# Kernel optimization log

Hardware: AMD Instinct MI355X
Metric: run time of the kernel (lower is better)

The kernel has to match this reference:

```python
import jax, jax.numpy as jnp
import numpy as np

NUM_USERS = 4000
NUM_LOCAS = 4000
D = 128            # embedding_dynamic_size
K = 64             # kg embedding dim
KG_ROWS = 5000
T = 2048           # number of events
IN_RNN = D + 1 + K # rnn input size (KG=True)
PRED_IN = NUM_USERS + NUM_LOCAS + 2 * D + K
PRED_OUT = NUM_LOCAS + D + K
EPS = 1e-12


def setup_inputs() -> dict:
    key = jax.random.key(0)
    ks = jax.random.split(key, 20)
    s = 0.05
    f32 = jnp.float32
    return {
        "embedding": jax.random.normal(ks[0], (NUM_USERS + NUM_LOCAS, D), f32),
        "events_int": jax.random.randint(ks[1], (T, 5), 0, 4000, dtype=jnp.int32),
        "delta_u": jax.random.uniform(ks[2], (T,), f32),
        "delta_l": jax.random.uniform(ks[3], (T,), f32),
        "kg": jax.random.normal(ks[4], (KG_ROWS, K), f32) * s,
        "w_ih_u": jax.random.normal(ks[5], (D, IN_RNN), f32) * s,
        "w_hh_u": jax.random.normal(ks[6], (D, D), f32) * s,
        "b_ih_u": jax.random.normal(ks[7], (D,), f32) * s,
        "b_hh_u": jax.random.normal(ks[8], (D,), f32) * s,
        "w_ih_l": jax.random.normal(ks[9], (D, IN_RNN), f32) * s,
        "w_hh_l": jax.random.normal(ks[10], (D, D), f32) * s,
        "b_ih_l": jax.random.normal(ks[11], (D,), f32) * s,
        "b_hh_l": jax.random.normal(ks[12], (D,), f32) * s,
        "proj_w": jax.random.normal(ks[13], (D, 1), f32) * s,
        "proj_b": jax.random.normal(ks[14], (D,), f32) * s,
        "pred_w": jax.random.normal(ks[15], (PRED_OUT, PRED_IN), f32) * s,
        "pred_b": jax.random.normal(ks[16], (PRED_OUT,), f32) * s,
    }


def _l2norm(x):
    # F.normalize(dim=-1) on a single row
    n = jnp.sqrt(jnp.sum(x * x))
    return x / jnp.maximum(n, EPS)


def reference(embedding, events_int, delta_u, delta_l, kg,
              w_ih_u, w_hh_u, b_ih_u, b_hh_u,
              w_ih_l, w_hh_l, b_ih_l, b_hh_l,
              proj_w, proj_b, pred_w, pred_b):
    # split prediction weight columns to match concat order:
    # [proj_user(D), emb_prev(D), kg_prev(K), static_loca(one-hot L), static_user(one-hot U)]
    W_proj_in = pred_w[:, :D]
    W_prev = pred_w[:, D:2 * D]
    W_kgp = pred_w[:, 2 * D:2 * D + K]
    W_sl = pred_w[:, 2 * D + K:2 * D + K + NUM_LOCAS]
    W_su = pred_w[:, 2 * D + K + NUM_LOCAS:]
    pw = proj_w[:, 0]

    def step(carry, ev):
        emb, loss = carry
        idx, du, dl = ev
        u, loca, prev, know_prev, know = idx[0], idx[1], idx[2], idx[3], idx[4]
        loca_g = loca + NUM_USERS
        prev_g = prev + NUM_USERS
        e_u = emb[u]        # [D]
        e_l = emb[loca_g]   # [D]
        e_p = emb[prev_g]   # [D]

        # projection: emb_user * (1 + Linear(1->D)(delta_u))
        proj = e_u * (1.0 + pw * du + proj_b)

        # prediction (one-hot static blocks -> column selects)
        pred = (W_proj_in @ proj + W_prev @ e_p + W_kgp @ kg[know_prev]
                + W_sl[:, prev] + W_su[:, u] + pred_b)
        one_hot_prev = jax.nn.one_hot(prev, NUM_LOCAS, dtype=emb.dtype)
        target = jax.lax.stop_gradient(
            jnp.concatenate([e_l, one_hot_prev, kg[know]]))
        loss = loss + jnp.mean((pred - target) ** 2)

        # RNNCell updates (tanh), inputs use pre-update embeddings
        inp_u = jnp.concatenate([e_l, kg[know], du[None]])
        new_u = _l2norm(jnp.tanh(w_ih_u @ inp_u + b_ih_u + w_hh_u @ e_u + b_hh_u))
        inp_l = jnp.concatenate([e_u, kg[know], dl[None]])
        new_l = _l2norm(jnp.tanh(w_ih_l @ inp_l + b_ih_l + w_hh_l @ e_l + b_hh_l))

        loss = loss + jnp.mean((new_u - jax.lax.stop_gradient(e_u)) ** 2)
        loss = loss + jnp.mean((new_l - jax.lax.stop_gradient(e_l)) ** 2)

        emb = emb.at[u].set(new_u).at[loca_g].set(new_l)
        return (emb, loss), None

    (emb_out, loss), _ = jax.lax.scan(
        step, (embedding, jnp.zeros((), embedding.dtype)),
        (events_int, delta_u, delta_l))
    return emb_out, loss
```

## Files before the change

### kernel.cpp

```cpp
#include <hip/hip_runtime.h>

#define T_STEPS 2048
#define NUSERS 4000
#define NLOCAS 4000
#define DD 128
#define KK 64
#define PRED_OUT 4192
#define PRED_IN 8256
#define OUT_EMB 1024000
#define TAIL_LV 8
#define WB_ROWS 4224

typedef __attribute__((ext_vector_type(8))) short short8v;
typedef __attribute__((ext_vector_type(4))) float f32x4;

#define WS_NEWU   0
#define WS_NEWL   262144
#define WS_KU     524288
#define WS_KL     786432
#define WS_ZB     1048576
#define WS_WB     1376256
#define WS_ELT    2052096
#define WS_DRIFT  2314240
#define WS_ROWP   2316288
#define WS_INT    2450432
#define WS_S      2464832
#define IO_PU     0
#define IO_PL     2048
#define IO_PP     4096
#define IO_LASTU  6144
#define IO_LASTL  8192
#define IO_ORDER  10240
#define IO_OFF    12288
#define IO_NLEV   14337

__device__ inline unsigned short f2bf(float f) {
    unsigned int x = __float_as_uint(f);
    unsigned int r = (x + 0x7FFFu + ((x >> 16) & 1u)) >> 16;
    return (unsigned short)r;
}

__global__ __launch_bounds__(256) void init_kernel(const float* __restrict__ emb_in,
                                                   float* __restrict__ out) {
    int i = blockIdx.x * blockDim.x + threadIdx.x;
    int stride = gridDim.x * blockDim.x;
    for (; i < OUT_EMB; i += stride) out[i] = emb_in[i];
}

__global__ __launch_bounds__(256) void preds_kernel(const int* __restrict__ ev,
                                                    int* __restrict__ ibase) {
    __shared__ int su[T_STEPS];
    __shared__ int sl[T_STEPS];
    const int tid  = threadIdx.x;
    const int lane = tid & 63;
    const int wid  = tid >> 6;
    for (int i = tid; i < T_STEPS; i += 256) { su[i] = ev[i*5]; sl[i] = ev[i*5+1]; }
    __syncthreads();

    const int t = blockIdx.x * 4 + wid;
    const int u = su[t], l = sl[t], p = ev[t*5 + 2];

    int pu = -1, pl = -1, pp = -1;
    {
        int round = 0;
        while (true) {
            const int q = t - 1 - lane - (round << 6);
            const int squ = (q >= 0) ? su[q] : -1;
            const int sql = (q >= 0) ? sl[q] : -1;
            if (pu < 0) {
                unsigned long long b = __ballot(squ == u);
                if (b) pu = t - 1 - (__ffsll(b) - 1) - (round << 6);
            }
            if (pl < 0) {
                unsigned long long b = __ballot(sql == l);
                if (b) pl = t - 1 - (__ffsll(b) - 1) - (round << 6);
            }
            if (pp < 0) {
                unsigned long long b = __ballot(sql == p);
                if (b) pp = t - 1 - (__ffsll(b) - 1) - (round << 6);
            }
            ++round;
            if ((pu >= 0 && pl >= 0 && pp >= 0) || (t - 1 - (round << 6) < 0)) break;
        }
    }

    int lastu = 1, lastl = 1;
    {
        int round = 0;
        while (true) {
            const int q = t + 1 + lane + (round << 6);
            const int squ = (q < T_STEPS) ? su[q] : -1;
            const int sql = (q < T_STEPS) ? sl[q] : -1;
            if (lastu && __ballot(squ == u)) lastu = 0;
            if (lastl && __ballot(sql == l)) lastl = 0;
            ++round;
            if ((!lastu && !lastl) || (t + 1 + (round << 6) >= T_STEPS)) break;
        }
    }

    if (lane == 0) {
        ibase[IO_PU + t] = pu;
        ibase[IO_PL + t] = pl;
        ibase[IO_PP + t] = pp;
        ibase[IO_LASTU + t] = lastu;
        ibase[IO_LASTL + t] = lastl;
    }
}

__global__ __launch_bounds__(1024) void levels_kernel(int* __restrict__ ibase) {
    __shared__ int lev[T_STEPS];
    __shared__ int spu[T_STEPS];
    __shared__ int spl[T_STEPS];
    __shared__ int cnt[T_STEPS + 1];
    __shared__ int changed;
    __shared__ int smax;
    const int tid = threadIdx.x;

    for (int i = tid; i < T_STEPS; i += 1024) {
        spu[i] = ibase[IO_PU + i];
        spl[i] = ibase[IO_PL + i];
        lev[i] = 0;
    }
    if (tid == 0) smax = 0;
    __syncthreads();

    while (true) {
        if (tid == 0) changed = 0;
        __syncthreads();
        for (int i = tid; i < T_STEPS; i += 1024) {
            int nl = 0, a = spu[i], b = spl[i];
            if (a >= 0) nl = lev[a] + 1;
            if (b >= 0) { int v = lev[b] + 1; if (v > nl) nl = v; }
            if (nl > lev[i]) { lev[i] = nl; changed = 1; }
        }
        __syncthreads();
        if (!changed) break;
        __syncthreads();
    }

    for (int i = tid; i <= T_STEPS; i += 1024) cnt[i] = 0;
    __syncthreads();
    for (int i = tid; i < T_STEPS; i += 1024) {
        atomicAdd(&cnt[lev[i]], 1);
        atomicMax(&smax, lev[i]);
    }
    __syncthreads();
    if (tid == 0) {
        int nlev = smax + 1;
        int acc = 0;
        for (int k = 0; k < nlev; ++k) {
            ibase[IO_OFF + k] = acc;
            int c = cnt[k]; cnt[k] = acc; acc += c;
        }
        ibase[IO_OFF + nlev] = acc;
        ibase[IO_NLEV] = nlev;
        for (int k = nlev + 1; k <= TAIL_LV; ++k) ibase[IO_OFF + k] = acc;
    }
    __syncthreads();
    for (int i = tid; i < T_STEPS; i += 1024) {
        int pos = atomicAdd(&cnt[lev[i]], 1);
        ibase[IO_ORDER + pos] = i;
    }
}

__global__ __launch_bounds__(128) void precomp_k(const int* __restrict__ ev,
    const float* __restrict__ du, const float* __restrict__ dl,
    const float* __restrict__ kg,
    const float* __restrict__ wihu, const float* __restrict__ bihu, const float* __restrict__ bhhu,
    const float* __restrict__ wihl, const float* __restrict__ bihl, const float* __restrict__ bhhl,
    float* __restrict__ KU, float* __restrict__ KL) {
    int t = blockIdx.x;
    int r = threadIdx.x;
    __shared__ float skg[KK];
    int kn = ev[t*5 + 4];
    if (r < KK) skg[r] = kg[kn*KK + r];
    __syncthreads();
    float dut = du[t], dlt = dl[t];
    const float* wu = wihu + r*193;
    const float* wl = wihl + r*193;
    float ku = bihu[r] + bhhu[r] + wu[192]*dut;
    float kl = bihl[r] + bhhl[r] + wl[192]*dlt;
    #pragma unroll
    for (int j = 0; j < KK; ++j) {
        float s = skg[j];
        ku += wu[128+j]*s;
        kl += wl[128+j]*s;
    }
    KU[t*DD + r] = ku;
    KL[t*DD + r] = kl;
}

__global__ __launch_bounds__(512) void chain_sweep(int lv, const int* __restrict__ ev,
    const float* __restrict__ emb0,
    const float* __restrict__ wihu, const float* __restrict__ whhu,
    const float* __restrict__ whhl, const float* __restrict__ wihl,
    const float* __restrict__ KU, const float* __restrict__ KL,
    float* __restrict__ NEWU, float* __restrict__ NEWL, float* __restrict__ DRIFT,
    const int* __restrict__ ibase) {
    const int start = ibase[IO_OFF + lv];
    const int end   = ibase[IO_OFF + lv + 1];
    if ((int)blockIdx.x >= end - start) return;

    const int tid  = threadIdx.x;
    const int h    = tid >> 8;
    const int r    = tid & 255;
    const int lane = tid & 63;
    const int wid  = tid >> 6;

    float w[128];
    {
        const float* src;
        if (h == 0) src = (r < 128) ? (wihu + r*193) : (whhl + (r-128)*128);
        else        src = (r < 128) ? (whhu + r*128) : (wihl + (r-128)*193);
        #pragma unroll
        for (int j = 0; j < 128; ++j) w[j] = src[j];
    }

    __shared__ float xs[256];
    __shared__ float partial[512];
    __shared__ float wsum[8];

    for (int s = start + blockIdx.x; s < end; s += gridDim.x) {
        const int t  = ibase[IO_ORDER + s];
        const int u  = ev[t*5];
        const int l  = ev[t*5 + 1];
        const int pu = ibase[IO_PU + t];
        const int pl = ibase[IO_PL + t];

        float kv = 0.f;
        if (tid < 128) {
            xs[tid] = (pl >= 0) ? NEWL[pl*DD + tid] : emb0[(size_t)(l + NUSERS)*DD + tid];
            kv = KU[t*DD + tid];
        } else if (tid < 256) {
            int d = tid - 128;
            xs[tid] = (pu >= 0) ? NEWU[pu*DD + d] : emb0[(size_t)u*DD + d];
            kv = KL[t*DD + d];
        }
        __syncthreads();

        float acc = 0.f;
        {
            const float* xp = xs + h*128;
            #pragma unroll
            for (int j = 0; j < 128; ++j) acc += w[j] * xp[j];
        }
        partial[tid] = acc;
        __syncthreads();

        float th = 0.f;
        if (tid < 256) {
            float pre = partial[tid] + partial[256 + tid] + kv;
            th = tanhf(pre);
            float ss = th * th;
            #pragma unroll
            for (int o = 32; o > 0; o >>= 1) ss += __shfl_xor(ss, o, 64);
            if (lane == 0) wsum[wid] = ss;
        }
        __syncthreads();

        if (tid < 256) {
            float S  = (tid < 128) ? (wsum[0] + wsum[1]) : (wsum[2] + wsum[3]);
            float sf = 1.f / fmaxf(sqrtf(S), 1e-12f);
            float v2 = th * sf;
            float old = (tid < 128) ? xs[128 + tid] : xs[tid - 128];
            if (tid < 128) NEWU[t*DD + tid]       = v2;
            else           NEWL[t*DD + (tid-128)] = v2;
            float dd = v2 - old;
            float s2 = dd * dd;
            #pragma unroll
            for (int o = 32; o > 0; o >>= 1) s2 += __shfl_xor(s2, o, 64);
            if (lane == 0) wsum[4 + wid] = s2;
        }
        __syncthreads();
        if (tid == 0)
            DRIFT[t] = (wsum[4] + wsum[5] + wsum[6] + wsum[7]) * (1.f / 128.f);
    }
}

__global__ __launch_bounds__(512) void chain_tail(const int* __restrict__ ev,
    const float* __restrict__ emb0,
    const float* __restrict__ wihu, const float* __restrict__ whhu,
    const float* __restrict__ whhl, const float* __restrict__ wihl,
    const float* __restrict__ KU, const float* __restrict__ KL,
    float* __restrict__ NEWU, float* __restrict__ NEWL, float* __restrict__ DRIFT,
    const int* __restrict__ ibase) {
    const int nlev = ibase[IO_NLEV];
    if (nlev <= TAIL_LV) return;
    const int start = ibase[IO_OFF + TAIL_LV];
    const int end   = ibase[IO_OFF + nlev];

    const int tid  = threadIdx.x;
    const int h    = tid >> 8;
    const int r    = tid & 255;
    const int lane = tid & 63;
    const int wid  = tid >> 6;

    float w[128];
    {
        const float* src;
        if (h == 0) src = (r < 128) ? (wihu + r*193) : (whhl + (r-128)*128);
        else        src = (r < 128) ? (whhu + r*128) : (wihl + (r-128)*193);
        #pragma unroll
        for (int j = 0; j < 128; ++j) w[j] = src[j];
    }

    __shared__ float xs[256];
    __shared__ float partial[512];
    __shared__ float wsum[8];

    for (int s = start; s < end; ++s) {
        const int t  = ibase[IO_ORDER + s];
        const int u  = ev[t*5];
        const int l  = ev[t*5 + 1];
        const int pu = ibase[IO_PU + t];
        const int pl = ibase[IO_PL + t];

        float kv = 0.f;
        if (tid < 128) {
            xs[tid] = (pl >= 0) ? NEWL[pl*DD + tid] : emb0[(size_t)(l + NUSERS)*DD + tid];
            kv = KU[t*DD + tid];
        } else if (tid < 256) {
            int d = tid - 128;
            xs[tid] = (pu >= 0) ? NEWU[pu*DD + d] : emb0[(size_t)u*DD + d];
            kv = KL[t*DD + d];
        }
        __syncthreads();

        float acc = 0.f;
        {
            const float* xp = xs + h*128;
            #pragma unroll
            for (int j = 0; j < 128; ++j) acc += w[j] * xp[j];
        }
        partial[tid] = acc;
        __syncthreads();

        float th = 0.f;
        if (tid < 256) {
            float pre = partial[tid] + partial[256 + tid] + kv;
            th = tanhf(pre);
            float ss = th * th;
            #pragma unroll
            for (int o = 32; o > 0; o >>= 1) ss += __shfl_xor(ss, o, 64);
            if (lane == 0) wsum[wid] = ss;
        }
        __syncthreads();

        if (tid < 256) {
            float S  = (tid < 128) ? (wsum[0] + wsum[1]) : (wsum[2] + wsum[3]);
            float sf = 1.f / fmaxf(sqrtf(S), 1e-12f);
            float v2 = th * sf;
            float old = (tid < 128) ? xs[128 + tid] : xs[tid - 128];
            if (tid < 128) NEWU[t*DD + tid]       = v2;
            else           NEWL[t*DD + (tid-128)] = v2;
            float dd = v2 - old;
            float s2 = dd * dd;
            #pragma unroll
            for (int o = 32; o > 0; o >>= 1) s2 += __shfl_xor(s2, o, 64);
            if (lane == 0) wsum[4 + wid] = s2;
        }
        __syncthreads();
        if (tid == 0)
            DRIFT[t] = (wsum[4] + wsum[5] + wsum[6] + wsum[7]) * (1.f / 128.f);
    }
}

__global__ __launch_bounds__(256) void build_z(const int* __restrict__ ev,
    const float* __restrict__ emb0, const float* __restrict__ du,
    const float* __restrict__ pw, const float* __restrict__ projb,
    const float* __restrict__ kg,
    const float* __restrict__ NEWU, const float* __restrict__ NEWL,
    unsigned short* __restrict__ Zb, float* __restrict__ ELT,
    float* __restrict__ out, const int* __restrict__ ibase) {
    const int gsz = gridDim.x * blockDim.x;
    const int gid = blockIdx.x * blockDim.x + threadIdx.x;

    for (int i = gid; i < T_STEPS*320; i += gsz) {
        int t = i / 320, j = i - t*320;
        float zv;
        if (j < 128) {
            int pu = ibase[IO_PU + t];
            int uu = ev[t*5];
            float eu = (pu >= 0) ? NEWU[pu*DD + j] : emb0[(size_t)uu*DD + j];
            zv = eu * (1.f + pw[j]*du[t] + projb[j]);
        } else if (j < 256) {
            int jj = j - 128;
            int pp = ibase[IO_PP + t];
            int pv = ev[t*5 + 2];
            zv = (pp >= 0) ? NEWL[pp*DD + jj] : emb0[(size_t)(pv + NUSERS)*DD + jj];
        } else {
            int kp = ev[t*5 + 3];
            zv = kg[kp*KK + (j - 256)];
        }
        Zb[i] = f2bf(zv);
    }
    for (int i = gid; i < DD*T_STEPS; i += gsz) {
        int d = i >> 11, t = i & 2047;
        int pl = ibase[IO_PL + t];
        int l  = ev[t*5 + 1];
        ELT[i] = (pl >= 0) ? NEWL[pl*DD + d] : emb0[(size_t)(l + NUSERS)*DD + d];
    }
    for (int i = gid; i < T_STEPS*DD; i += gsz) {
        int t = i >> 7, d = i & 127;
        if (ibase[IO_LASTU + t]) out[(size_t)ev[t*5]*DD + d]            = NEWU[i];
        if (ibase[IO_LASTL + t]) out[(size_t)(ev[t*5+1]+NUSERS)*DD + d] = NEWL[i];
    }
}

__global__ __launch_bounds__(256) void convw(const float* __restrict__ predw,
                                             unsigned short* __restrict__ Wb) {
    const int gsz = gridDim.x * blockDim.x;
    for (int i = blockIdx.x * blockDim.x + threadIdx.x; i < WB_ROWS*80; i += gsz) {
        int r = i / 80, kc = (i - r*80) * 4;
        unsigned short o0 = 0, o1 = 0, o2 = 0, o3 = 0;
        if (r < PRED_OUT) {
            const float4 v = *(const float4*)(predw + (size_t)r*PRED_IN + kc);
            o0 = f2bf(v.x); o1 = f2bf(v.y); o2 = f2bf(v.z); o3 = f2bf(v.w);
        }
        unsigned short* dst = Wb + (size_t)r*320 + kc;
        dst[0] = o0; dst[1] = o1; dst[2] = o2; dst[3] = o3;
    }
}

__global__ __launch_bounds__(256) void pred_dense_mfma(
    const unsigned short* __restrict__ Wb, const unsigned short* __restrict__ Zb,
    float* __restrict__ S, int NT, int t0) {
    const int tid = threadIdx.x;
    const int l   = tid & 63;
    const int w   = tid >> 6;
    const int wr  = w >> 1, wc = w & 1;
    const int lr  = l & 15;
    const int kg8 = (l >> 4) * 8;
    const int r0  = blockIdx.y * 128 + wr * 64;
    const int tt0 = blockIdx.x * 128 + wc * 64;

    f32x4 acc[4][4];
    #pragma unroll
    for (int m = 0; m < 4; ++m)
        #pragma unroll
        for (int n = 0; n < 4; ++n) acc[m][n] = (f32x4){0.f, 0.f, 0.f, 0.f};

    for (int k0 = 0; k0 < 320; k0 += 32) {
        short8v a[4], b[4];
        #pragma unroll
        for (int m = 0; m < 4; ++m)
            a[m] = *(const short8v*)(Wb + (size_t)(r0 + m*16 + lr)*320 + k0 + kg8);
        #pragma unroll
        for (int n = 0; n < 4; ++n)
            b[n] = *(const short8v*)(Zb + (size_t)(t0 + tt0 + n*16 + lr)*320 + k0 + kg8);
        #pragma unroll
        for (int m = 0; m < 4; ++m)
            #pragma unroll
            for (int n = 0; n < 4; ++n)
                acc[m][n] = __builtin_amdgcn_mfma_f32_16x16x32_bf16(a[m], b[n], acc[m][n], 0, 0, 0);
    }

    const int orow = (l >> 4) * 4;
    #pragma unroll
    for (int m = 0; m < 4; ++m) {
        #pragma unroll
        for (int i = 0; i < 4; ++i) {
            int r = r0 + m*16 + orow + i;
            if (r < PRED_OUT) {
                float* dst = S + (size_t)r*NT + tt0 + lr;
                #pragma unroll
                for (int n = 0; n < 4; ++n) dst[n*16] = acc[m][n][i];
            }
        }
    }
}

__global__ __launch_bounds__(256) void pred_scatter(const int* __restrict__ ev,
    const float* __restrict__ predw, const float* __restrict__ predb,
    const float* __restrict__ kg, const float* __restrict__ S,
    const float* __restrict__ ELT, float* __restrict__ rowp,
    int NT, int t0, int chunk) {
    __shared__ float srow[NLOCAS + NUSERS];
    __shared__ float red[4];
    const int tid = threadIdx.x;
    const int lane = tid & 63, wid = tid >> 6;
    const int r = blockIdx.x;
    const float* base = predw + (size_t)r*PRED_IN + 320;
    #pragma unroll
    for (int i = 0; i < 8; ++i) {
        int idx = (tid + i*256) * 4;
        if (idx < NLOCAS + NUSERS) {
            float4 v = *(const float4*)(base + idx);
            *(float4*)(srow + idx) = v;
        }
    }
    __syncthreads();
    const float bias = predb[r];
    const int mode = (r < DD) ? 0 : (r < DD + NLOCAS ? 1 : 2);
    float lsum = 0.f;
    for (int tloc = tid; tloc < NT; tloc += 256) {
        int t = t0 + tloc;
        int pv = ev[t*5 + 2];
        int uu = ev[t*5 + 0];
        float v = S[(size_t)r*NT + tloc] + bias + srow[pv] + srow[NLOCAS + uu];
        float tv;
        if (mode == 0)      tv = ELT[r*T_STEPS + t];
        else if (mode == 1) tv = (pv == r - DD) ? 1.f : 0.f;
        else                tv = kg[ev[t*5+4]*KK + (r - DD - NLOCAS)];
        float d = v - tv;
        lsum += d*d;
    }
    #pragma unroll
    for (int o = 32; o > 0; o >>= 1) lsum += __shfl_xor(lsum, o, 64);
    if (lane == 0) red[wid] = lsum;
    __syncthreads();
    if (tid == 0) rowp[chunk*PRED_OUT + r] = red[0] + red[1] + red[2] + red[3];
}

__global__ __launch_bounds__(256) void final_reduce(const float* __restrict__ rowp,
                                                    const float* __restrict__ drift,
                                                    float* __restrict__ out, int nchunk) {
    int tid = threadIdx.x;
    float s = 0.f;
    for (int i = tid; i < nchunk*PRED_OUT; i += 256) s += rowp[i];
    s *= (1.0f / PRED_OUT);
    for (int i = tid; i < T_STEPS; i += 256) s += drift[i];
    #pragma unroll
    for (int o = 32; o > 0; o >>= 1) s += __shfl_xor(s, o, 64);
    __shared__ float red[4];
    if ((tid & 63) == 0) red[tid >> 6] = s;
    __syncthreads();
    if (tid == 0) out[OUT_EMB] = red[0] + red[1] + red[2] + red[3];
}

extern "C" void kernel_launch(void* const* d_in, const int* in_sizes, int n_in,
                              void* d_out, int out_size, void* d_ws, size_t ws_size,
                              hipStream_t stream) {
    const float* emb_in = (const float*)d_in[0];
    const int*   ev     = (const int*)  d_in[1];
    const float* du     = (const float*)d_in[2];
    const float* dl     = (const float*)d_in[3];
    const float* kg     = (const float*)d_in[4];
    const float* wihu   = (const float*)d_in[5];
    const float* whhu   = (const float*)d_in[6];
    const float* bihu   = (const float*)d_in[7];
    const float* bhhu   = (const float*)d_in[8];
    const float* wihl   = (const float*)d_in[9];
    const float* whhl   = (const float*)d_in[10];
    const float* bihl   = (const float*)d_in[11];
    const float* bhhl   = (const float*)d_in[12];
    const float* projw  = (const float*)d_in[13];
    const float* projb  = (const float*)d_in[14];
    const float* predw  = (const float*)d_in[15];
    const float* predb  = (const float*)d_in[16];

    float* out = (float*)d_out;
    float* ws  = (float*)d_ws;
    float* NEWU  = ws + WS_NEWU;
    float* NEWL  = ws + WS_NEWL;
    float* KU    = ws + WS_KU;
    float* KL    = ws + WS_KL;
    unsigned short* Zb = (unsigned short*)(ws + WS_ZB);
    unsigned short* Wb = (unsigned short*)(ws + WS_WB);
    float* ELT   = ws + WS_ELT;
    float* DRIFT = ws + WS_DRIFT;
    float* ROWP  = ws + WS_ROWP;
    float* S     = ws + WS_S;
    int*   ibase = (int*)(ws + WS_INT);

    long avail = (long)(ws_size / 4) - WS_S;
    int NT = 2048;
    while (NT > 128 && (long)PRED_OUT * NT > avail) NT >>= 1;
    int nchunk = T_STEPS / NT;

    init_kernel<<<2048, 256, 0, stream>>>(emb_in, out);
    preds_kernel<<<T_STEPS/4, 256, 0, stream>>>(ev, ibase);
    levels_kernel<<<1, 1024, 0, stream>>>(ibase);
    precomp_k<<<T_STEPS, 128, 0, stream>>>(ev, du, dl, kg, wihu, bihu, bhhu,
                                           wihl, bihl, bhhl, KU, KL);
    convw<<<1320, 256, 0, stream>>>(predw, Wb);
    for (int lv = 0; lv < TAIL_LV; ++lv)
        chain_sweep<<<256, 512, 0, stream>>>(lv, ev, emb_in, wihu, whhu, whhl, wihl,
                                             KU, KL, NEWU, NEWL, DRIFT, ibase);
    chain_tail<<<1, 512, 0, stream>>>(ev, emb_in, wihu, whhu, whhl, wihl,
                                      KU, KL, NEWU, NEWL, DRIFT, ibase);
    build_z<<<1024, 256, 0, stream>>>(ev, emb_in, du, projw, projb, kg,
                                      NEWU, NEWL, Zb, ELT, out, ibase);
    for (int c = 0; c < nchunk; ++c) {
        int t0 = c * NT;
        pred_dense_mfma<<<dim3(NT/128, 33), 256, 0, stream>>>(Wb, Zb, S, NT, t0);
        pred_scatter<<<PRED_OUT, 256, 0, stream>>>(ev, predw, predb, kg, S, ELT,
                                                   ROWP, NT, t0, c);
    }
    final_reduce<<<1, 256, 0, stream>>>(ROWP, DRIFT, out, nchunk);
}
```

Before: 211.7 us.

## Fuse prep kernels into one launch and vectorize weight and S loads

Merges the embedding copy, previous-occurrence search, KU/KL precompute and bf16 weight conversion into a single heterogeneous prep kernel split by block index. This removes three launches and lets the independent prep tasks run concurrently. Chain kernels now load weight rows with float4, and pred_scatter reads S four elements at a time. The float4 loads on rows with stride 193 are misaligned, which relies on the hardware tolerating unaligned vector loads.

```diff
diff --git a/kernel.cpp b/kernel.cpp
--- a/kernel.cpp
+++ b/kernel.cpp
@@ -40,70 +40,115 @@
     return (unsigned short)r;
 }
 
-__global__ __launch_bounds__(256) void init_kernel(const float* __restrict__ emb_in,
-                                                   float* __restrict__ out) {
-    int i = blockIdx.x * blockDim.x + threadIdx.x;
-    int stride = gridDim.x * blockDim.x;
-    for (; i < OUT_EMB; i += stride) out[i] = emb_in[i];
-}
-
-__global__ __launch_bounds__(256) void preds_kernel(const int* __restrict__ ev,
-                                                    int* __restrict__ ibase) {
+__global__ __launch_bounds__(256) void prep_kernel(const int* __restrict__ ev,
+    const float* __restrict__ emb_in, const float* __restrict__ du,
+    const float* __restrict__ dl, const float* __restrict__ kg,
+    const float* __restrict__ wihu, const float* __restrict__ bihu,
+    const float* __restrict__ bhhu, const float* __restrict__ wihl,
+    const float* __restrict__ bihl, const float* __restrict__ bhhl,
+    const float* __restrict__ predw,
+    float* __restrict__ out, float* __restrict__ KU, float* __restrict__ KL,
+    unsigned short* __restrict__ Wb, int* __restrict__ ibase) {
     __shared__ int su[T_STEPS];
     __shared__ int sl[T_STEPS];
-    const int tid  = threadIdx.x;
-    const int lane = tid & 63;
-    const int wid  = tid >> 6;
-    for (int i = tid; i < T_STEPS; i += 256) { su[i] = ev[i*5]; sl[i] = ev[i*5+1]; }
-    __syncthreads();
-
-    const int t = blockIdx.x * 4 + wid;
-    const int u = su[t], l = sl[t], p = ev[t*5 + 2];
-
-    int pu = -1, pl = -1, pp = -1;
-    {
-        int round = 0;
-        while (true) {
-            const int q = t - 1 - lane - (round << 6);
-            const int squ = (q >= 0) ? su[q] : -1;
-            const int sql = (q >= 0) ? sl[q] : -1;
-            if (pu < 0) {
-                unsigned long long b = __ballot(squ == u);
-                if (b) pu = t - 1 - (__ffsll(b) - 1) - (round << 6);
+    __shared__ float skg[4][KK];
+    __shared__ int kn4[4];
+    const int tid = threadIdx.x;
+
+    if (blockIdx.x < 512) {
+        const int lane = tid & 63;
+        const int wid  = tid >> 6;
+        for (int i = tid; i < T_STEPS; i += 256) { su[i] = ev[i*5]; sl[i] = ev[i*5+1]; }
+        __syncthreads();
+
+        const int t = blockIdx.x * 4 + wid;
+        const int u = su[t], l = sl[t], p = ev[t*5 + 2];
+
+        int pu = -1, pl = -1, pp = -1;
+        {
+            int round = 0;
+            while (true) {
+                const int q = t - 1 - lane - (round << 6);
+                const int squ = (q >= 0) ? su[q] : -1;
+                const int sql = (q >= 0) ? sl[q] : -1;
+                if (pu < 0) {
+                    unsigned long long b = __ballot(squ == u);
+                    if (b) pu = t - 1 - (__ffsll(b) - 1) - (round << 6);
+                }
+                if (pl < 0) {
+                    unsigned long long b = __ballot(sql == l);
+                    if (b) pl = t - 1 - (__ffsll(b) - 1) - (round << 6);
+                }
+                if (pp < 0) {
+                    unsigned long long b = __ballot(sql == p);
+                    if (b) pp = t - 1 - (__ffsll(b) - 1) - (round << 6);
+                }
+                ++round;
+                if ((pu >= 0 && pl >= 0 && pp >= 0) || (t - 1 - (round << 6) < 0)) break;
             }
-            if (pl < 0) {
-                unsigned long long b = __ballot(sql == l);
-                if (b) pl = t - 1 - (__ffsll(b) - 1) - (round << 6);
+        }
+        int lastu = 1, lastl = 1;
+        {
+            int round = 0;
+            while (true) {
+                const int q = t + 1 + lane + (round << 6);
+                const int squ = (q < T_STEPS) ? su[q] : -1;
+                const int sql = (q < T_STEPS) ? sl[q] : -1;
+                if (lastu && __ballot(squ == u)) lastu = 0;
+                if (lastl && __ballot(sql == l)) lastl = 0;
+                ++round;
+                if ((!lastu && !lastl) || (t + 1 + (round << 6) >= T_STEPS)) break;
             }
-            if (pp < 0) {
-                unsigned long long b = __ballot(sql == p);
-                if (b) pp = t - 1 - (__ffsll(b) - 1) - (round << 6);
-            }
-            ++round;
-            if ((pu >= 0 && pl >= 0 && pp >= 0) || (t - 1 - (round << 6) < 0)) break;
-        }
-    }
-
-    int lastu = 1, lastl = 1;
-    {
-        int round = 0;
-        while (true) {
-            const int q = t + 1 + lane + (round << 6);
-            const int squ = (q < T_STEPS) ? su[q] : -1;
-            const int sql = (q < T_STEPS) ? sl[q] : -1;
-            if (lastu && __ballot(squ == u)) lastu = 0;
-            if (lastl && __ballot(sql == l)) lastl = 0;
-            ++round;
-            if ((!lastu && !lastl) || (t + 1 + (round << 6) >= T_STEPS)) break;
-        }
-    }
-
-    if (lane == 0) {
-        ibase[IO_PU + t] = pu;
-        ibase[IO_PL + t] = pl;
-        ibase[IO_PP + t] = pp;
-        ibase[IO_LASTU + t] = lastu;
-        ibase[IO_LASTL + t] = lastl;
+        }
+        if (lane == 0) {
+            ibase[IO_PU + t] = pu;
+            ibase[IO_PL + t] = pl;
+            ibase[IO_PP + t] = pp;
+            ibase[IO_LASTU + t] = lastu;
+            ibase[IO_LASTL + t] = lastl;
+        }
+        return;
+    }
+
+    const int pb = blockIdx.x - 512;
+    if (tid < 4) kn4[tid] = ev[(pb*4 + tid)*5 + 4];
+    __syncthreads();
+    skg[tid >> 6][tid & 63] = kg[kn4[tid >> 6]*KK + (tid & 63)];
+    __syncthreads();
+    #pragma unroll
+    for (int p = 0; p < 2; ++p) {
+        const int sub = p*2 + (tid >> 7);
+        const int t = pb*4 + sub;
+        const int r = tid & 127;
+        const float* wu = wihu + r*193;
+        const float* wl = wihl + r*193;
+        const float dut = du[t], dlt = dl[t];
+        float ku = bihu[r] + bhhu[r] + wu[192]*dut;
+        float kl = bihl[r] + bhhl[r] + wl[192]*dlt;
+        const float* sk = skg[sub];
+        #pragma unroll
+        for (int j = 0; j < KK; ++j) {
+            float s = sk[j];
+            ku += wu[128+j]*s;
+            kl += wl[128+j]*s;
+        }
+        KU[t*DD + r] = ku;
+        KL[t*DD + r] = kl;
+    }
+
+    const int gsz = 512 * 256;
+    const int gid = pb * 256 + tid;
+    for (int i = gid; i < OUT_EMB/4; i += gsz)
+        ((float4*)out)[i] = ((const float4*)emb_in)[i];
+    for (int i = gid; i < WB_ROWS*80; i += gsz) {
+        int r = i / 80, kc = (i - r*80) * 4;
+        unsigned short o0 = 0, o1 = 0, o2 = 0, o3 = 0;
+        if (r < PRED_OUT) {
+            const float4 v = *(const float4*)(predw + (size_t)r*PRED_IN + kc);
+            o0 = f2bf(v.x); o1 = f2bf(v.y); o2 = f2bf(v.z); o3 = f2bf(v.w);
+        }
+        unsigned short* dst = Wb + (size_t)r*320 + kc;
+        dst[0] = o0; dst[1] = o1; dst[2] = o2; dst[3] = o3;
     }
 }
 
@@ -161,33 +206,6 @@
         int pos = atomicAdd(&cnt[lev[i]], 1);
         ibase[IO_ORDER + pos] = i;
     }
-}
-
-__global__ __launch_bounds__(128) void precomp_k(const int* __restrict__ ev,
-    const float* __restrict__ du, const float* __restrict__ dl,
-    const float* __restrict__ kg,
-    const float* __restrict__ wihu, const float* __restrict__ bihu, const float* __restrict__ bhhu,
-    const float* __restrict__ wihl, const float* __restrict__ bihl, const float* __restrict__ bhhl,
-    float* __restrict__ KU, float* __restrict__ KL) {
-    int t = blockIdx.x;
-    int r = threadIdx.x;
-    __shared__ float skg[KK];
-    int kn = ev[t*5 + 4];
-    if (r < KK) skg[r] = kg[kn*KK + r];
-    __syncthreads();
-    float dut = du[t], dlt = dl[t];
-    const float* wu = wihu + r*193;
-    const float* wl = wihl + r*193;
-    float ku = bihu[r] + bhhu[r] + wu[192]*dut;
-    float kl = bihl[r] + bhhl[r] + wl[192]*dlt;
-    #pragma unroll
-    for (int j = 0; j < KK; ++j) {
-        float s = skg[j];
-        ku += wu[128+j]*s;
-        kl += wl[128+j]*s;
-    }
-    KU[t*DD + r] = ku;
-    KL[t*DD + r] = kl;
 }
 
 __global__ __launch_bounds__(512) void chain_sweep(int lv, const int* __restrict__ ev,
@@ -213,7 +231,10 @@
         if (h == 0) src = (r < 128) ? (wihu + r*193) : (whhl + (r-128)*128);
         else        src = (r < 128) ? (whhu + r*128) : (wihl + (r-128)*193);
         #pragma unroll
-        for (int j = 0; j < 128; ++j) w[j] = src[j];
+        for (int j = 0; j < 32; ++j) {
+            const float4 v = *(const float4*)(src + j*4);
+            w[j*4+0] = v.x; w[j*4+1] = v.y; w[j*4+2] = v.z; w[j*4+3] = v.w;
+        }
     }
 
     __shared__ float xs[256];
@@ -301,7 +322,10 @@
         if (h == 0) src = (r < 128) ? (wihu + r*193) : (whhl + (r-128)*128);
         else        src = (r < 128) ? (whhu + r*128) : (wihl + (r-128)*193);
         #pragma unroll
-        for (int j = 0; j < 128; ++j) w[j] = src[j];
+        for (int j = 0; j < 32; ++j) {
+            const float4 v = *(const float4*)(src + j*4);
+            w[j*4+0] = v.x; w[j*4+1] = v.y; w[j*4+2] = v.z; w[j*4+3] = v.w;
+        }
     }
 
     __shared__ float xs[256];
@@ -404,21 +428,6 @@
         int t = i >> 7, d = i & 127;
         if (ibase[IO_LASTU + t]) out[(size_t)ev[t*5]*DD + d]            = NEWU[i];
         if (ibase[IO_LASTL + t]) out[(size_t)(ev[t*5+1]+NUSERS)*DD + d] = NEWL[i];
-    }
-}
-
-__global__ __launch_bounds__(256) void convw(const float* __restrict__ predw,
-                                             unsigned short* __restrict__ Wb) {
-    const int gsz = gridDim.x * blockDim.x;
-    for (int i = blockIdx.x * blockDim.x + threadIdx.x; i < WB_ROWS*80; i += gsz) {
-        int r = i / 80, kc = (i - r*80) * 4;
-        unsigned short o0 = 0, o1 = 0, o2 = 0, o3 = 0;
-        if (r < PRED_OUT) {
-            const float4 v = *(const float4*)(predw + (size_t)r*PRED_IN + kc);
-            o0 = f2bf(v.x); o1 = f2bf(v.y); o2 = f2bf(v.z); o3 = f2bf(v.w);
-        }
-        unsigned short* dst = Wb + (size_t)r*320 + kc;
-        dst[0] = o0; dst[1] = o1; dst[2] = o2; dst[3] = o3;
     }
 }
 
@@ -493,17 +502,22 @@
     const float bias = predb[r];
     const int mode = (r < DD) ? 0 : (r < DD + NLOCAS ? 1 : 2);
     float lsum = 0.f;
-    for (int tloc = tid; tloc < NT; tloc += 256) {
-        int t = t0 + tloc;
-        int pv = ev[t*5 + 2];
-        int uu = ev[t*5 + 0];
-        float v = S[(size_t)r*NT + tloc] + bias + srow[pv] + srow[NLOCAS + uu];
-        float tv;
-        if (mode == 0)      tv = ELT[r*T_STEPS + t];
-        else if (mode == 1) tv = (pv == r - DD) ? 1.f : 0.f;
-        else                tv = kg[ev[t*5+4]*KK + (r - DD - NLOCAS)];
-        float d = v - tv;
-        lsum += d*d;
+    for (int tb = tid*4; tb < NT; tb += 1024) {
+        const float4 sv = *(const float4*)(S + (size_t)r*NT + tb);
+        const float sa[4] = {sv.x, sv.y, sv.z, sv.w};
+        #pragma unroll
+        for (int q = 0; q < 4; ++q) {
+            int t = t0 + tb + q;
+            int pv = ev[t*5 + 2];
+            int uu = ev[t*5 + 0];
+            float v = sa[q] + bias + srow[pv] + srow[NLOCAS + uu];
+            float tv;
+            if (mode == 0)      tv = ELT[r*T_STEPS + t];
+            else if (mode == 1) tv = (pv == r - DD) ? 1.f : 0.f;
+            else                tv = kg[ev[t*5+4]*KK + (r - DD - NLOCAS)];
+            float d = v - tv;
+            lsum += d*d;
+        }
     }
     #pragma unroll
     for (int o = 32; o > 0; o >>= 1) lsum += __shfl_xor(lsum, o, 64);
@@ -568,12 +582,10 @@
     while (NT > 128 && (long)PRED_OUT * NT > avail) NT >>= 1;
     int nchunk = T_STEPS / NT;
 
-    init_kernel<<<2048, 256, 0, stream>>>(emb_in, out);
-    preds_kernel<<<T_STEPS/4, 256, 0, stream>>>(ev, ibase);
+    prep_kernel<<<1024, 256, 0, stream>>>(ev, emb_in, du, dl, kg,
+                                          wihu, bihu, bhhu, wihl, bihl, bhhl,
+                                          predw, out, KU, KL, Wb, ibase);
     levels_kernel<<<1, 1024, 0, stream>>>(ibase);
-    precomp_k<<<T_STEPS, 128, 0, stream>>>(ev, du, dl, kg, wihu, bihu, bhhu,
-                                           wihl, bihl, bhhl, KU, KL);
-    convw<<<1320, 256, 0, stream>>>(predw, Wb);
     for (int lv = 0; lv < TAIL_LV; ++lv)
         chain_sweep<<<256, 512, 0, stream>>>(lv, ev, emb_in, wihu, whhu, whhl, wihl,
                                              KU, KL, NEWU, NEWL, DRIFT, ibase);
```

Result: faster. 204.3 us (-3.5%).
